# Kernel tuning notes

Measured on AMD Instinct MI355X. Metric: run time of the kernel, lower is better.

Reference implementation:

```python
import jax, jax.numpy as jnp
import numpy as np

B, S, D = 4, 2048, 512
H, KD, VD = 8, 64, 64


def glorot(key, shape):
    fan_in, fan_out = shape[-2], shape[-1]
    limit = np.sqrt(6.0 / (fan_in + fan_out)).astype(np.float32)
    return jax.random.uniform(key, shape, jnp.float32, -limit, limit)


def setup_inputs() -> dict:
    key = jax.random.key(0)
    ks = jax.random.split(key, 6)
    input_tensor = jax.random.normal(ks[0], (B, S, D), jnp.float32)
    input_mask = jnp.ones((B, S), jnp.float32)
    # Per-head projections stacked along a leading head axis [H, D, kd/vd]
    Wq = glorot(ks[1], (H, D, KD))
    Wk = glorot(ks[2], (H, D, KD))
    Wv = glorot(ks[3], (H, D, VD))
    Wo = glorot(ks[4], (H * VD, VD))
    # dot_product_scales initialized to 1 in the original (tf.Variable(1))
    scales = jnp.ones((H,), jnp.float32)
    return {"input_tensor": input_tensor, "input_mask": input_mask,
            "Wq": Wq, "Wk": Wk, "Wv": Wv, "Wo": Wo, "scales": scales}


def reference(input_tensor, input_mask, Wq, Wk, Wv, Wo, scales):
    # Vectorized over the original per-head Python loop (identical math).
    q = jnp.einsum('bsd,hdk->bhsk', input_tensor, Wq)
    k = jnp.einsum('bsd,hdk->bhsk', input_tensor, Wk)
    v = jnp.einsum('bsd,hdv->bhsv', input_tensor, Wv)
    # dotproduct notation 'bik,bjk->bij' per head, scaled by per-head scale
    scores = jnp.einsum('bhik,bhjk->bhij', q, k) * scales[None, :, None, None]
    # reshape to [..., -1] then softmax == softmax over last (key) axis here
    attn = jax.nn.softmax(scores, axis=-1)
    # kv notation 'bij,bjv,bi,bj->biv' with the mask applied twice
    ctx = jnp.einsum('bhij,bhjv,bi,bj->bhiv', attn, v, input_mask, input_mask)
    # concat heads along last axis (head-major order, as in the loop)
    ctx = jnp.transpose(ctx, (0, 2, 1, 3)).reshape(ctx.shape[0], ctx.shape[2], -1)
    return ctx @ Wo
```

## Files before the change

kernel.cpp:

```cpp
#include <hip/hip_runtime.h>
#include <hip/hip_bf16.h>


typedef _Float16 f16x8 __attribute__((ext_vector_type(8)));
typedef float    f32x4  __attribute__((ext_vector_type(4)));
typedef float    f32x16 __attribute__((ext_vector_type(16)));
typedef __fp16   hf2 __attribute__((ext_vector_type(2)));

#define BB 4
#define SS 2048
#define DD 512
#define HH 8
#define KDIM 64
#define NSPLIT 2
#define TPS 16

#define EXP2F(x) __builtin_amdgcn_exp2f(x)

#define GLOAD_LDS16(gp, lp)                                                   \
  __builtin_amdgcn_global_load_lds(                                          \
      (const __attribute__((address_space(1))) void*)(gp),                    \
      (__attribute__((address_space(3))) void*)(lp), 16, 0, 0)

#define SWZ(row, bc) ((row) * 128 + ((bc) ^ (((row) & 7) << 4)))

static __device__ __forceinline__ unsigned pk2(float a, float b) {
  auto h = __builtin_amdgcn_cvt_pkrtz(a, b);
  return __builtin_bit_cast(unsigned, h);
}

union PU { unsigned u[4]; f16x8 v; };

__global__ __launch_bounds__(256) void convert_x(
    const float* __restrict__ x, _Float16* __restrict__ xf) {
  size_t i = ((size_t)blockIdx.x * 256 + threadIdx.x) * 8;
  float4 a = *(const float4*)&x[i];
  float4 b = *(const float4*)&x[i + 4];
  float vv[8] = {a.x, a.y, a.z, a.w, b.x, b.y, b.z, b.w};
  _Float16 hb[8];
#pragma unroll
  for (int u = 0; u < 8; ++u) hb[u] = (_Float16)vv[u];
  *(uint4*)&xf[i] = *(uint4*)hb;
}

__global__ __launch_bounds__(256) void convert_w(
    const float* __restrict__ Wq, const float* __restrict__ Wk,
    const float* __restrict__ Wv, _Float16* __restrict__ wtf) {
  __shared__ float s_tile[64][65];
  const int t = threadIdx.x;
  const int kb = blockIdx.x;
  const int hw = blockIdx.y;
  const int which = hw >> 3, h = hw & 7;
  const float* W = (which == 0) ? Wq : (which == 1) ? Wk : Wv;
  const float* src = W + (size_t)h * DD * KDIM + (size_t)kb * 64 * KDIM;

  {
    int kk = t >> 2, c0 = (t & 3) * 16;
#pragma unroll
    for (int u = 0; u < 4; ++u)
      *(float4*)&s_tile[kk][c0 + u * 4] = *(const float4*)&src[kk * KDIM + c0 + u * 4];
  }
  __syncthreads();

  int kd = t >> 2, kk0 = (t & 3) * 16;
  int n = which * 512 + h * 64 + kd;
  _Float16 hb[16];
#pragma unroll
  for (int u = 0; u < 16; ++u) hb[u] = (_Float16)s_tile[kk0 + u][kd];
  size_t off = (size_t)n * DD + kb * 64 + kk0;
  *(uint4*)&wtf[off] = *(uint4*)&hb[0];
  *(uint4*)&wtf[off + 8] = *(uint4*)&hb[8];
}

__global__ __launch_bounds__(256) void convert_wo(
    const float* __restrict__ Wo, _Float16* __restrict__ woT) {
  __shared__ float s_tile[64][65];
  const int t = threadIdx.x;
  const int kb = blockIdx.x;
  const float* src = Wo + (size_t)kb * 64 * 64;
  {
    int kk = t >> 2, c0 = (t & 3) * 16;
#pragma unroll
    for (int u = 0; u < 4; ++u)
      *(float4*)&s_tile[kk][c0 + u * 4] = *(const float4*)&src[kk * 64 + c0 + u * 4];
  }
  __syncthreads();
  int col = t >> 2, kk0 = (t & 3) * 16;
  _Float16 hb[16];
#pragma unroll
  for (int u = 0; u < 16; ++u) hb[u] = (_Float16)s_tile[kk0 + u][col];
  size_t off = (size_t)col * DD + kb * 64 + kk0;
  *(uint4*)&woT[off] = *(uint4*)&hb[0];
  *(uint4*)&woT[off + 8] = *(uint4*)&hb[8];
}

__global__ __launch_bounds__(256) void qkv_gemm(
    const _Float16* __restrict__ xf, const _Float16* __restrict__ wtf,
    const float* __restrict__ mask, const float* __restrict__ scales,
    _Float16* __restrict__ qf, _Float16* __restrict__ kf,
    _Float16* __restrict__ vT) {
  __shared__ _Float16 Af[128 * 32], Bf[128 * 32];
  const int t = threadIdx.x, l = t & 63, w = t >> 6;
  const int wr = w >> 1, wc = w & 1;
  const int m0 = blockIdx.y * 128, n0 = blockIdx.x * 128;

  f32x4 acc[4][4];
#pragma unroll
  for (int m = 0; m < 4; ++m)
#pragma unroll
    for (int n = 0; n < 4; ++n) acc[m][n] = f32x4{0.f, 0.f, 0.f, 0.f};

  const int rl = l >> 2, ce = (l & 3) * 8;

  for (int kt = 0; kt < 16; ++kt) {
    const int k0 = kt * 32;
    __syncthreads();
#pragma unroll
    for (int i = 0; i < 2; ++i) {
      const int row = w * 32 + i * 16;
      const size_t aoff = (size_t)(m0 + row + rl) * DD + k0 + ce;
      const size_t boff = (size_t)(n0 + row + rl) * DD + k0 + ce;
      GLOAD_LDS16(xf + aoff, &Af[row * 32]);
      GLOAD_LDS16(wtf + boff, &Bf[row * 32]);
    }
    __syncthreads();

    f16x8 ah[4], bh[4];
#pragma unroll
    for (int m = 0; m < 4; ++m) {
      int r = wr * 64 + m * 16 + (l & 15);
      ah[m] = *(const f16x8*)&Af[r * 32 + (l >> 4) * 8];
    }
#pragma unroll
    for (int n = 0; n < 4; ++n) {
      int r = wc * 64 + n * 16 + (l & 15);
      bh[n] = *(const f16x8*)&Bf[r * 32 + (l >> 4) * 8];
    }
#pragma unroll
    for (int m = 0; m < 4; ++m)
#pragma unroll
      for (int n = 0; n < 4; ++n)
        acc[m][n] = __builtin_amdgcn_mfma_f32_16x16x32_f16(ah[m], bh[n], acc[m][n], 0, 0, 0);
  }

#pragma unroll
  for (int n = 0; n < 4; ++n) {
    int colg = n0 + wc * 64 + n * 16 + (l & 15);
    int which = colg >> 9, rem = colg & 511;
    int h = rem >> 6, kd = rem & 63;
    float qsc = (which == 0) ? scales[h] * 1.44269504f : 1.f;
#pragma unroll
    for (int m = 0; m < 4; ++m) {
      int row0 = m0 + wr * 64 + m * 16 + (l >> 4) * 4;
      if (which == 2) {
        int b = row0 >> 11, s0 = row0 & 2047;
        _Float16 tmp[4] __attribute__((aligned(8)));
#pragma unroll
        for (int j = 0; j < 4; ++j)
          tmp[j] = (_Float16)(acc[m][n][j] * mask[row0 + j]);
        *(uint2*)&vT[((size_t)(b * HH + h) * KDIM + kd) * SS + s0] = *(uint2*)tmp;
      } else {
        _Float16* dst = (which == 0) ? qf : kf;
#pragma unroll
        for (int j = 0; j < 4; ++j) {
          int row = row0 + j;
          int b = row >> 11, s = row & 2047;
          dst[(((size_t)b * HH + h) * SS + s) * KDIM + kd] =
              (_Float16)(acc[m][n][j] * qsc);
        }
      }
    }
  }
}

__global__ __launch_bounds__(256) void attn_kernel(
    const _Float16* __restrict__ qg, const _Float16* __restrict__ kg,
    const _Float16* __restrict__ vTg,
    _Float16* __restrict__ po, float* __restrict__ pli) {
  const int t = threadIdx.x;
  const int l = t & 63, w = t >> 6;
  const int lr = l & 31, hi = l >> 5;
  const int bh = blockIdx.y;
  const int q0 = blockIdx.x * 128;
  const int split = blockIdx.z;

  __shared__ _Float16 ksf[2][64 * 64];
  __shared__ _Float16 vts[2][64 * 64];

  const size_t base = (size_t)bh * SS * KDIM;
  const size_t vbase = (size_t)bh * KDIM * SS;

  const int srow = l >> 3;
  const int ecol = ((l & 7) * 8) ^ ((srow & 7) * 8);

  f16x8 qfr[4];
  const int s_q = q0 + w * 32 + lr;
#pragma unroll
  for (int kb = 0; kb < 4; ++kb)
    qfr[kb] = *(const f16x8*)&qg[base + (size_t)s_q * KDIM + kb * 16 + hi * 8];

  float m_s = -1e30f, lsum = 0.f;
  f32x16 oacc[2] = {};

  const int kt0 = split * TPS;

#pragma unroll
  for (int c = 0; c < 2; ++c) {
    const int r = w * 16 + c * 8 + srow;
    GLOAD_LDS16(kg + base + (size_t)(kt0 * 64 + r) * KDIM + ecol,
                &ksf[0][(w * 16 + c * 8) * 64]);
    GLOAD_LDS16(vTg + vbase + (size_t)r * SS + kt0 * 64 + ecol,
                &vts[0][(w * 16 + c * 8) * 64]);
  }
  __syncthreads();

  for (int tt = 0; tt < TPS; ++tt) {
    const int cur = tt & 1;
    if (tt + 1 < TPS) {
      const int ktn = kt0 + tt + 1;
#pragma unroll
      for (int c = 0; c < 2; ++c) {
        const int r = w * 16 + c * 8 + srow;
        GLOAD_LDS16(kg + base + (size_t)(ktn * 64 + r) * KDIM + ecol,
                    &ksf[1 - cur][(w * 16 + c * 8) * 64]);
        GLOAD_LDS16(vTg + vbase + (size_t)r * SS + ktn * 64 + ecol,
                    &vts[1 - cur][(w * 16 + c * 8) * 64]);
      }
    }

    f32x16 st2[2];
#pragma unroll
    for (int jb = 0; jb < 2; ++jb) {
      f32x16 acc = {};
      const int krow = jb * 32 + lr;
#pragma unroll
      for (int kb = 0; kb < 4; ++kb) {
        f16x8 kfr = *(const f16x8*)((const char*)&ksf[cur][0] + SWZ(krow, kb * 32 + hi * 16));
        acc = __builtin_amdgcn_mfma_f32_32x32x16_f16(kfr, qfr[kb], acc, 0, 0, 0);
      }
      st2[jb] = acc;
    }

    float m8[8];
#pragma unroll
    for (int i = 0; i < 8; ++i)
      m8[i] = fmaxf(fmaxf(st2[0][i], st2[0][i + 8]),
                    fmaxf(st2[1][i], st2[1][i + 8]));
    float m4a = fmaxf(m8[0], m8[1]), m4b = fmaxf(m8[2], m8[3]);
    float m4c = fmaxf(m8[4], m8[5]), m4d = fmaxf(m8[6], m8[7]);
    float mt = fmaxf(fmaxf(m4a, m4b), fmaxf(m4c, m4d));
    mt = fmaxf(mt, __shfl_xor(mt, 32, 64));

    if (!__all(mt <= m_s + 11.5f)) {
      float mn = fmaxf(m_s, mt);
      float rs = EXP2F(m_s - mn);
      m_s = mn;
      lsum *= rs;
#pragma unroll
      for (int nb = 0; nb < 2; ++nb)
#pragma unroll
        for (int rr = 0; rr < 16; ++rr) oacc[nb][rr] *= rs;
    }

    float ps0 = 0.f, ps1 = 0.f;
    unsigned wds[2][4][2];
#pragma unroll
    for (int jb = 0; jb < 2; ++jb)
#pragma unroll
      for (int g = 0; g < 4; ++g) {
        float p0 = EXP2F(st2[jb][g * 4 + 0] - m_s);
        float p1 = EXP2F(st2[jb][g * 4 + 1] - m_s);
        float p2 = EXP2F(st2[jb][g * 4 + 2] - m_s);
        float p3 = EXP2F(st2[jb][g * 4 + 3] - m_s);
        unsigned pa = pk2(p0, p1), pb = pk2(p2, p3);
        wds[jb][g][0] = pa;
        wds[jb][g][1] = pb;
#if __has_builtin(__builtin_amdgcn_fdot2)
        hf2 one2 = {(__fp16)1.f, (__fp16)1.f};
        ps0 = __builtin_amdgcn_fdot2(__builtin_bit_cast(hf2, pa), one2, ps0, false);
        ps1 = __builtin_amdgcn_fdot2(__builtin_bit_cast(hf2, pb), one2, ps1, false);
#else
        ps0 += p0 + p1;
        ps1 += p2 + p3;
#endif
      }
    float psum = ps0 + ps1;
    psum += __shfl_xor(psum, 32, 64);
    lsum += psum;

#pragma unroll
    for (int kb = 0; kb < 4; ++kb) {
      const int jb = kb >> 1, gb = (kb & 1) * 2;
      unsigned s0 = hi ? wds[jb][gb][0] : wds[jb][gb + 1][0];
      unsigned s1 = hi ? wds[jb][gb][1] : wds[jb][gb + 1][1];
      unsigned r0 = (unsigned)__shfl_xor((int)s0, 32, 64);
      unsigned r1 = (unsigned)__shfl_xor((int)s1, 32, 64);
      PU pu;
      pu.u[0] = hi ? r0 : wds[jb][gb][0];
      pu.u[1] = hi ? r1 : wds[jb][gb][1];
      pu.u[2] = hi ? wds[jb][gb + 1][0] : r0;
      pu.u[3] = hi ? wds[jb][gb + 1][1] : r1;
#pragma unroll
      for (int nb = 0; nb < 2; ++nb) {
        f16x8 vf = *(const f16x8*)((const char*)&vts[cur][0] + SWZ(nb * 32 + lr, kb * 32 + hi * 16));
        oacc[nb] = __builtin_amdgcn_mfma_f32_32x32x16_f16(vf, pu.v, oacc[nb], 0, 0, 0);
      }
    }

    __syncthreads();
  }

  const float inv = 1.0f / lsum;
  const float li = m_s + __log2f(lsum);
  _Float16* prow = po + (((size_t)split * (BB * HH) + bh) * SS + s_q) * KDIM;
#pragma unroll
  for (int nb = 0; nb < 2; ++nb)
#pragma unroll
    for (int g = 0; g < 4; ++g) {
      uint2 o;
      o.x = pk2(oacc[nb][g * 4 + 0] * inv, oacc[nb][g * 4 + 1] * inv);
      o.y = pk2(oacc[nb][g * 4 + 2] * inv, oacc[nb][g * 4 + 3] * inv);
      *(uint2*)&prow[nb * 32 + g * 8 + hi * 4] = o;
    }
  if (hi == 0)
    pli[((size_t)split * (BB * HH) + bh) * SS + s_q] = li;
}

__global__ __launch_bounds__(256) void attn_combine(
    const _Float16* __restrict__ po, const float* __restrict__ pli,
    const float* __restrict__ mask, _Float16* __restrict__ ctxf) {
  const int t = threadIdx.x;
  const int row = blockIdx.x * 32 + (t >> 3);
  const int c = t & 7;
  const int bh = row >> 11, qrow = row & 2047;
  const int b = bh >> 3, h = bh & 7;
  const int NR = BB * HH * SS;

  float li[NSPLIT];
#pragma unroll
  for (int s = 0; s < NSPLIT; ++s) li[s] = pli[(size_t)s * NR + row];
  float L = li[0];
#pragma unroll
  for (int s = 1; s < NSPLIT; ++s) L = fmaxf(L, li[s]);
  float wgt[NSPLIT], wsum = 0.f;
#pragma unroll
  for (int s = 0; s < NSPLIT; ++s) { wgt[s] = EXP2F(li[s] - L); wsum += wgt[s]; }

  float acc[8] = {};
#pragma unroll
  for (int s = 0; s < NSPLIT; ++s) {
    uint4 u = *(const uint4*)&po[((size_t)s * NR + row) * KDIM + c * 8];
    const _Float16* hp = (const _Float16*)&u;
#pragma unroll
    for (int j = 0; j < 8; ++j) acc[j] += wgt[s] * (float)hp[j];
  }
  const float sc = mask[b * SS + qrow] / wsum;
  _Float16 ob[8] __attribute__((aligned(16)));
#pragma unroll
  for (int j = 0; j < 8; ++j) ob[j] = (_Float16)(acc[j] * sc);
  *(uint4*)&ctxf[((size_t)b * SS + qrow) * (HH * KDIM) + h * KDIM + c * 8] =
      *(uint4*)ob;
}

__global__ __launch_bounds__(256) void oproj_gemm(
    const _Float16* __restrict__ ctxf, const _Float16* __restrict__ woT,
    float* __restrict__ out) {
  __shared__ _Float16 Af[64 * 32], Bf[64 * 32];
  const int t = threadIdx.x, l = t & 63, w = t >> 6;
  const int lr = l & 31, hi = l >> 5;
  const int wr = w >> 1, wc = w & 1;
  const size_t rowbase = (size_t)blockIdx.x * 64;
  const int rl = l >> 2, ce = (l & 3) * 8;

  f32x16 acc = {};
  for (int kt = 0; kt < 16; ++kt) {
    const int k0 = kt * 32;
    __syncthreads();
    {
      const int row = w * 16;
      GLOAD_LDS16(ctxf + (rowbase + row + rl) * DD + k0 + ce, &Af[row * 32]);
      GLOAD_LDS16(woT + (size_t)(row + rl) * DD + k0 + ce, &Bf[row * 32]);
    }
    __syncthreads();
#pragma unroll
    for (int ks = 0; ks < 2; ++ks) {
      f16x8 af = *(const f16x8*)&Af[(wr * 32 + lr) * 32 + ks * 16 + hi * 8];
      f16x8 bf = *(const f16x8*)&Bf[(wc * 32 + lr) * 32 + ks * 16 + hi * 8];
      acc = __builtin_amdgcn_mfma_f32_32x32x16_f16(af, bf, acc, 0, 0, 0);
    }
  }
#pragma unroll
  for (int rr = 0; rr < 16; ++rr) {
    int m = (rr & 3) + 8 * (rr >> 2) + 4 * hi;
    out[(rowbase + wr * 32 + m) * 64 + wc * 32 + lr] = acc[rr];
  }
}

extern "C" void kernel_launch(void* const* d_in, const int* in_sizes, int n_in,
                              void* d_out, int out_size, void* d_ws, size_t ws_size,
                              hipStream_t stream) {
  const float* x     = (const float*)d_in[0];
  const float* mask  = (const float*)d_in[1];
  const float* Wq    = (const float*)d_in[2];
  const float* Wk    = (const float*)d_in[3];
  const float* Wv    = (const float*)d_in[4];
  const float* Wo    = (const float*)d_in[5];
  const float* scales= (const float*)d_in[6];
  float* out = (float*)d_out;

  char* ws = (char*)d_ws;
  const size_t xb  = (size_t)BB * SS * DD * sizeof(_Float16);
  const size_t wb  = (size_t)3 * 512 * DD * sizeof(_Float16);
  const size_t wob = (size_t)64 * DD * sizeof(_Float16);
  const size_t qb  = (size_t)BB * HH * SS * KDIM * sizeof(_Float16);
  const size_t pob = (size_t)NSPLIT * BB * HH * SS * KDIM * sizeof(_Float16);

  _Float16* xfb  = (_Float16*)(ws);
  _Float16* wtfb = (_Float16*)(ws + xb);
  _Float16* woTb = (_Float16*)(ws + xb + wb);
  char* p = ws + xb + wb + wob;
  _Float16* qfb  = (_Float16*)(p);
  _Float16* kfb  = (_Float16*)(p + qb);
  _Float16* vTb  = (_Float16*)(p + 2 * qb);
  _Float16* ctxf = (_Float16*)(p + 3 * qb);
  _Float16* pob_p= (_Float16*)(p + 4 * qb);
  float*    pli_p= (float*)(p + 4 * qb + pob);
  (void)ws_size;

  convert_x<<<2048, 256, 0, stream>>>(x, xfb);
  convert_w<<<dim3(8, 24), 256, 0, stream>>>(Wq, Wk, Wv, wtfb);
  convert_wo<<<8, 256, 0, stream>>>(Wo, woTb);
  qkv_gemm<<<dim3(12, 64), 256, 0, stream>>>(xfb, wtfb, mask, scales,
                                             qfb, kfb, vTb);
  attn_kernel<<<dim3(SS / 128, BB * HH, NSPLIT), 256, 0, stream>>>(
      qfb, kfb, vTb, pob_p, pli_p);
  attn_combine<<<(BB * HH * SS) / 32, 256, 0, stream>>>(pob_p, pli_p, mask, ctxf);
  oproj_gemm<<<128, 256, 0, stream>>>(ctxf, woTb, out);
}
```

Baseline: 123.9 us.

## Process two query fragments per wave and double KV split count

After: 146.2 us. +18.0%, slower.

```diff
diff --git a/kernel.cpp b/kernel.cpp
--- a/kernel.cpp
+++ b/kernel.cpp
@@ -12,8 +12,8 @@
 #define DD 512
 #define HH 8
 #define KDIM 64
-#define NSPLIT 2
-#define TPS 16
+#define NSPLIT 4
+#define TPS 8
 
 #define EXP2F(x) __builtin_amdgcn_exp2f(x)
 
@@ -181,7 +181,7 @@
   const int l = t & 63, w = t >> 6;
   const int lr = l & 31, hi = l >> 5;
   const int bh = blockIdx.y;
-  const int q0 = blockIdx.x * 128;
+  const int q0 = blockIdx.x * 256;
   const int split = blockIdx.z;
 
   __shared__ _Float16 ksf[2][64 * 64];
@@ -193,14 +193,17 @@
   const int srow = l >> 3;
   const int ecol = ((l & 7) * 8) ^ ((srow & 7) * 8);
 
-  f16x8 qfr[4];
-  const int s_q = q0 + w * 32 + lr;
-#pragma unroll
-  for (int kb = 0; kb < 4; ++kb)
-    qfr[kb] = *(const f16x8*)&qg[base + (size_t)s_q * KDIM + kb * 16 + hi * 8];
-
-  float m_s = -1e30f, lsum = 0.f;
-  f32x16 oacc[2] = {};
+  f16x8 qfr[2][4];
+#pragma unroll
+  for (int f = 0; f < 2; ++f) {
+    const int s_qf = q0 + w * 64 + f * 32 + lr;
+#pragma unroll
+    for (int kb = 0; kb < 4; ++kb)
+      qfr[f][kb] = *(const f16x8*)&qg[base + (size_t)s_qf * KDIM + kb * 16 + hi * 8];
+  }
+
+  float m_s[2] = {-1e30f, -1e30f}, lsum[2] = {0.f, 0.f};
+  f32x16 oacc[2][2] = {};
 
   const int kt0 = split * TPS;
 
@@ -228,102 +231,125 @@
       }
     }
 
-    f32x16 st2[2];
+    f32x16 st[2][2];
+#pragma unroll
+    for (int f = 0; f < 2; ++f)
+#pragma unroll
+      for (int jb = 0; jb < 2; ++jb) st[f][jb] = f32x16{};
 #pragma unroll
     for (int jb = 0; jb < 2; ++jb) {
-      f32x16 acc = {};
       const int krow = jb * 32 + lr;
 #pragma unroll
       for (int kb = 0; kb < 4; ++kb) {
         f16x8 kfr = *(const f16x8*)((const char*)&ksf[cur][0] + SWZ(krow, kb * 32 + hi * 16));
-        acc = __builtin_amdgcn_mfma_f32_32x32x16_f16(kfr, qfr[kb], acc, 0, 0, 0);
-      }
-      st2[jb] = acc;
-    }
-
-    float m8[8];
-#pragma unroll
-    for (int i = 0; i < 8; ++i)
-      m8[i] = fmaxf(fmaxf(st2[0][i], st2[0][i + 8]),
-                    fmaxf(st2[1][i], st2[1][i + 8]));
-    float m4a = fmaxf(m8[0], m8[1]), m4b = fmaxf(m8[2], m8[3]);
-    float m4c = fmaxf(m8[4], m8[5]), m4d = fmaxf(m8[6], m8[7]);
-    float mt = fmaxf(fmaxf(m4a, m4b), fmaxf(m4c, m4d));
-    mt = fmaxf(mt, __shfl_xor(mt, 32, 64));
-
-    if (!__all(mt <= m_s + 11.5f)) {
-      float mn = fmaxf(m_s, mt);
-      float rs = EXP2F(m_s - mn);
-      m_s = mn;
-      lsum *= rs;
-#pragma unroll
-      for (int nb = 0; nb < 2; ++nb)
-#pragma unroll
-        for (int rr = 0; rr < 16; ++rr) oacc[nb][rr] *= rs;
-    }
-
-    float ps0 = 0.f, ps1 = 0.f;
-    unsigned wds[2][4][2];
-#pragma unroll
-    for (int jb = 0; jb < 2; ++jb)
-#pragma unroll
-      for (int g = 0; g < 4; ++g) {
-        float p0 = EXP2F(st2[jb][g * 4 + 0] - m_s);
-        float p1 = EXP2F(st2[jb][g * 4 + 1] - m_s);
-        float p2 = EXP2F(st2[jb][g * 4 + 2] - m_s);
-        float p3 = EXP2F(st2[jb][g * 4 + 3] - m_s);
-        unsigned pa = pk2(p0, p1), pb = pk2(p2, p3);
-        wds[jb][g][0] = pa;
-        wds[jb][g][1] = pb;
+        st[0][jb] = __builtin_amdgcn_mfma_f32_32x32x16_f16(kfr, qfr[0][kb], st[0][jb], 0, 0, 0);
+        st[1][jb] = __builtin_amdgcn_mfma_f32_32x32x16_f16(kfr, qfr[1][kb], st[1][jb], 0, 0, 0);
+      }
+    }
+
+#pragma unroll
+    for (int f = 0; f < 2; ++f) {
+      float m8[8];
+#pragma unroll
+      for (int i = 0; i < 8; ++i)
+        m8[i] = fmaxf(fmaxf(st[f][0][i], st[f][0][i + 8]),
+                      fmaxf(st[f][1][i], st[f][1][i + 8]));
+      float m4a = fmaxf(m8[0], m8[1]), m4b = fmaxf(m8[2], m8[3]);
+      float m4c = fmaxf(m8[4], m8[5]), m4d = fmaxf(m8[6], m8[7]);
+      float mt = fmaxf(fmaxf(m4a, m4b), fmaxf(m4c, m4d));
+      mt = fmaxf(mt, __shfl_xor(mt, 32, 64));
+      if (!__all(mt <= m_s[f] + 11.5f)) {
+        float mn = fmaxf(m_s[f], mt);
+        float rs = EXP2F(m_s[f] - mn);
+        m_s[f] = mn;
+        lsum[f] *= rs;
+#pragma unroll
+        for (int nb = 0; nb < 2; ++nb)
+#pragma unroll
+          for (int rr = 0; rr < 16; ++rr) oacc[f][nb][rr] *= rs;
+      }
+    }
+
+    unsigned wds[2][2][4][2];
+#pragma unroll
+    for (int f = 0; f < 2; ++f) {
+      float ps0 = 0.f, ps1 = 0.f;
+#pragma unroll
+      for (int jb = 0; jb < 2; ++jb)
+#pragma unroll
+        for (int g = 0; g < 4; ++g) {
+          float p0 = EXP2F(st[f][jb][g * 4 + 0] - m_s[f]);
+          float p1 = EXP2F(st[f][jb][g * 4 + 1] - m_s[f]);
+          float p2 = EXP2F(st[f][jb][g * 4 + 2] - m_s[f]);
+          float p3 = EXP2F(st[f][jb][g * 4 + 3] - m_s[f]);
+          unsigned pa = pk2(p0, p1), pb = pk2(p2, p3);
+          wds[f][jb][g][0] = pa;
+          wds[f][jb][g][1] = pb;
 #if __has_builtin(__builtin_amdgcn_fdot2)
-        hf2 one2 = {(__fp16)1.f, (__fp16)1.f};
-        ps0 = __builtin_amdgcn_fdot2(__builtin_bit_cast(hf2, pa), one2, ps0, false);
-        ps1 = __builtin_amdgcn_fdot2(__builtin_bit_cast(hf2, pb), one2, ps1, false);
+          hf2 one2 = {(__fp16)1.f, (__fp16)1.f};
+          ps0 = __builtin_amdgcn_fdot2(__builtin_bit_cast(hf2, pa), one2, ps0, false);
+          ps1 = __builtin_amdgcn_fdot2(__builtin_bit_cast(hf2, pb), one2, ps1, false);
 #else
-        ps0 += p0 + p1;
-        ps1 += p2 + p3;
+          ps0 += p0 + p1;
+          ps1 += p2 + p3;
 #endif
-      }
-    float psum = ps0 + ps1;
-    psum += __shfl_xor(psum, 32, 64);
-    lsum += psum;
-
+        }
+      float psum = ps0 + ps1;
+      psum += __shfl_xor(psum, 32, 64);
+      lsum[f] += psum;
+    }
+
+    unsigned rx[2][4][2];
 #pragma unroll
     for (int kb = 0; kb < 4; ++kb) {
       const int jb = kb >> 1, gb = (kb & 1) * 2;
-      unsigned s0 = hi ? wds[jb][gb][0] : wds[jb][gb + 1][0];
-      unsigned s1 = hi ? wds[jb][gb][1] : wds[jb][gb + 1][1];
-      unsigned r0 = (unsigned)__shfl_xor((int)s0, 32, 64);
-      unsigned r1 = (unsigned)__shfl_xor((int)s1, 32, 64);
-      PU pu;
-      pu.u[0] = hi ? r0 : wds[jb][gb][0];
-      pu.u[1] = hi ? r1 : wds[jb][gb][1];
-      pu.u[2] = hi ? wds[jb][gb + 1][0] : r0;
-      pu.u[3] = hi ? wds[jb][gb + 1][1] : r1;
-#pragma unroll
-      for (int nb = 0; nb < 2; ++nb) {
-        f16x8 vf = *(const f16x8*)((const char*)&vts[cur][0] + SWZ(nb * 32 + lr, kb * 32 + hi * 16));
-        oacc[nb] = __builtin_amdgcn_mfma_f32_32x32x16_f16(vf, pu.v, oacc[nb], 0, 0, 0);
+#pragma unroll
+      for (int f = 0; f < 2; ++f) {
+        unsigned s0 = hi ? wds[f][jb][gb][0] : wds[f][jb][gb + 1][0];
+        unsigned s1 = hi ? wds[f][jb][gb][1] : wds[f][jb][gb + 1][1];
+        rx[f][kb][0] = (unsigned)__shfl_xor((int)s0, 32, 64);
+        rx[f][kb][1] = (unsigned)__shfl_xor((int)s1, 32, 64);
+      }
+    }
+
+#pragma unroll
+    for (int kb = 0; kb < 4; ++kb) {
+      const int jb = kb >> 1, gb = (kb & 1) * 2;
+      f16x8 vf0 = *(const f16x8*)((const char*)&vts[cur][0] + SWZ(lr, kb * 32 + hi * 16));
+      f16x8 vf1 = *(const f16x8*)((const char*)&vts[cur][0] + SWZ(32 + lr, kb * 32 + hi * 16));
+#pragma unroll
+      for (int f = 0; f < 2; ++f) {
+        PU pu;
+        pu.u[0] = hi ? rx[f][kb][0] : wds[f][jb][gb][0];
+        pu.u[1] = hi ? rx[f][kb][1] : wds[f][jb][gb][1];
+        pu.u[2] = hi ? wds[f][jb][gb + 1][0] : rx[f][kb][0];
+        pu.u[3] = hi ? wds[f][jb][gb + 1][1] : rx[f][kb][1];
+        oacc[f][0] = __builtin_amdgcn_mfma_f32_32x32x16_f16(vf0, pu.v, oacc[f][0], 0, 0, 0);
+        oacc[f][1] = __builtin_amdgcn_mfma_f32_32x32x16_f16(vf1, pu.v, oacc[f][1], 0, 0, 0);
       }
     }
 
     __syncthreads();
   }
 
-  const float inv = 1.0f / lsum;
-  const float li = m_s + __log2f(lsum);
-  _Float16* prow = po + (((size_t)split * (BB * HH) + bh) * SS + s_q) * KDIM;
-#pragma unroll
-  for (int nb = 0; nb < 2; ++nb)
-#pragma unroll
-    for (int g = 0; g < 4; ++g) {
-      uint2 o;
-      o.x = pk2(oacc[nb][g * 4 + 0] * inv, oacc[nb][g * 4 + 1] * inv);
-      o.y = pk2(oacc[nb][g * 4 + 2] * inv, oacc[nb][g * 4 + 3] * inv);
-      *(uint2*)&prow[nb * 32 + g * 8 + hi * 4] = o;
-    }
-  if (hi == 0)
-    pli[((size_t)split * (BB * HH) + bh) * SS + s_q] = li;
+#pragma unroll
+  for (int f = 0; f < 2; ++f) {
+    const int s_qf = q0 + w * 64 + f * 32 + lr;
+    const float inv = 1.0f / lsum[f];
+    const float li = m_s[f] + __log2f(lsum[f]);
+    _Float16* prow = po + (((size_t)split * (BB * HH) + bh) * SS + s_qf) * KDIM;
+#pragma unroll
+    for (int nb = 0; nb < 2; ++nb)
+#pragma unroll
+      for (int g = 0; g < 4; ++g) {
+        uint2 o;
+        o.x = pk2(oacc[f][nb][g * 4 + 0] * inv, oacc[f][nb][g * 4 + 1] * inv);
+        o.y = pk2(oacc[f][nb][g * 4 + 2] * inv, oacc[f][nb][g * 4 + 3] * inv);
+        *(uint2*)&prow[nb * 32 + g * 8 + hi * 4] = o;
+      }
+    if (hi == 0)
+      pli[((size_t)split * (BB * HH) + bh) * SS + s_qf] = li;
+  }
 }
 
 __global__ __launch_bounds__(256) void attn_combine(
@@ -432,7 +458,7 @@
   convert_wo<<<8, 256, 0, stream>>>(Wo, woTb);
   qkv_gemm<<<dim3(12, 64), 256, 0, stream>>>(xfb, wtfb, mask, scales,
                                              qfb, kfb, vTb);
-  attn_kernel<<<dim3(SS / 128, BB * HH, NSPLIT), 256, 0, stream>>>(
+  attn_kernel<<<dim3(SS / 256, BB * HH, NSPLIT), 256, 0, stream>>>(
       qfb, kfb, vTb, pob_p, pli_p);
   attn_combine<<<(BB * HH * SS) / 32, 256, 0, stream>>>(pob_p, pli_p, mask, ctxf);
   oproj_gemm<<<128, 256, 0, stream>>>(ctxf, woTb, out);
```
